# Kernel optimization log

Hardware: AMD Instinct MI355X
Metric: run time of the kernel (lower is better)

The kernel has to match this reference:

```python
import math
import jax, jax.numpy as jnp
import numpy as np

B, N, E, R = 1024, 200, 256, 256

def _layernorm(x, g, b, eps=1e-5):
    mu = x.mean(-1, keepdims=True)
    var = ((x - mu) ** 2).mean(-1, keepdims=True)
    return (x - mu) / jnp.sqrt(var + eps) * g + b

def setup_inputs() -> dict:
    key = jax.random.key(0)
    ks = jax.random.split(key, 16)
    d = {}
    d["e_emb"] = jax.random.normal(ks[0], (B, E), jnp.float32)
    d["nb_rel"] = jax.random.normal(ks[1], (B, N, R), jnp.float32)
    d["delta_t"] = jax.random.uniform(ks[2], (B, N), jnp.float32) * 10.0
    d["r_emb"] = jax.random.normal(ks[3], (B, R), jnp.float32)
    d["hist_mask"] = jax.random.randint(ks[4], (B, N), 0, 2).astype(bool)
    d["rel_w"] = jax.random.normal(ks[5], (E, R), jnp.float32) / math.sqrt(R)
    d["log_tau1"] = jnp.asarray(1.0, jnp.float32)
    d["log_tau2"] = jnp.asarray(2.5, jnp.float32)
    d["sharpness"] = jnp.asarray(1.5, jnp.float32)
    d["log_gamma"] = jnp.asarray(-2.0, jnp.float32)
    d["attn_w"] = jax.random.normal(ks[6], (3, E, E), jnp.float32) / math.sqrt(E)
    d["sp_w"] = jax.random.normal(ks[7], (3, E, 6 * E), jnp.float32) / math.sqrt(6 * E)
    d["sp_b"] = jnp.zeros((3, E), jnp.float32)
    d["ln_g"] = jnp.ones((3, E), jnp.float32)
    d["ln_b"] = jnp.zeros((3, E), jnp.float32)
    d["csq_w"] = jax.random.normal(ks[8], (E, R), jnp.float32) / math.sqrt(R)
    d["csq_b"] = jnp.zeros((E,), jnp.float32)
    d["csl_w"] = jax.random.normal(ks[9], (3, E), jnp.float32) / math.sqrt(E)
    d["csl_b"] = jnp.zeros((3,), jnp.float32)
    d["on_g"] = jnp.ones((E,), jnp.float32)
    d["on_b"] = jnp.zeros((E,), jnp.float32)
    return d

def _pna_one_scale(msgs, mask, e_emb, q_key, attn_w, sp_w, sp_b, ln_g, ln_b):
    # msgs: [B,N,E], mask: [B,N] bool, e_emb: [B,E], q_key: [B,E]
    valid_f = mask[..., None].astype(msgs.dtype)
    n_valid = jnp.maximum(mask.astype(msgs.dtype).sum(1, keepdims=True), 1.0)  # [B,1]
    msgs_v = msgs * valid_f
    mean_v = msgs_v.sum(1) / n_valid
    max_v = msgs_v.max(1)
    min_v = jnp.clip(jnp.where(mask[..., None], msgs, 10000.0).min(1), -10000.0, 10000.0)
    sq_m = (jnp.clip(msgs_v, -10.0, 10.0) ** 2).sum(1) / n_valid
    std_v = jnp.sqrt(jnp.maximum(sq_m - mean_v ** 2, 1e-6))
    q_proj = q_key @ attn_w.T  # [B,E]
    attn_raw = jnp.einsum('bne,be->bn', msgs, q_proj) / math.sqrt(msgs.shape[-1])
    attn_raw = jnp.where(mask, attn_raw, -10000.0)
    all_invalid = ~mask.any(1, keepdims=True)  # [B,1]
    attn_raw = jnp.where(all_invalid, 0.0, attn_raw)
    attn_p = jax.nn.softmax(attn_raw, axis=-1)
    attn_v = jnp.einsum('bn,bne->be', attn_p, msgs)
    feats = jnp.concatenate([mean_v, max_v, min_v, std_v, attn_v, e_emb], axis=-1)  # [B,6E]
    h = feats @ sp_w.T + sp_b
    h = _layernorm(h, ln_g, ln_b)
    return jax.nn.gelu(h, approximate=False)  # dropout = identity (eval mode)

def reference(e_emb, nb_rel, delta_t, r_emb, hist_mask, rel_w, log_tau1, log_tau2,
              sharpness, log_gamma, attn_w, sp_w, sp_b, ln_g, ln_b,
              csq_w, csq_b, csl_w, csl_b, on_g, on_b):
    msgs = jnp.einsum('bnr,er->bne', nb_rel, rel_w)
    gamma = jnp.exp(log_gamma)
    decay = jnp.exp(-gamma * jnp.maximum(delta_t, 0.0))
    msgs_dec = msgs * decay[..., None]
    tau1 = jnp.exp(log_tau1)
    tau2 = jnp.exp(log_tau2) + tau1
    sharp = jnp.clip(sharpness, 0.1, 5.0)
    w_fine = jax.nn.sigmoid(-sharp * (delta_t - tau1))
    w_coarse = jax.nn.sigmoid(sharp * (delta_t - tau2))
    w_mid = jnp.maximum(1.0 - w_fine - w_coarse, 0.0)
    scale_w = jnp.stack([w_fine, w_mid, w_coarse])  # [3,B,N]
    m_scales = msgs_dec[None] * scale_w[..., None]  # [3,B,N,E]
    q_key = r_emb @ rel_w.T  # [B,E]
    pna_v = jax.vmap(_pna_one_scale, in_axes=(0, None, None, None, 0, 0, 0, 0, 0))
    scales = pna_v(m_scales, hist_mask, e_emb, q_key, attn_w, sp_w, sp_b, ln_g, ln_b)  # [3,B,E]
    sq = r_emb @ csq_w.T + csq_b  # [B,E]
    logits = sq @ csl_w.T + csl_b  # [B,3]
    weights = jax.nn.softmax(logits, axis=-1)
    out = jnp.einsum('bs,sbe->be', weights, scales)
    return _layernorm(out, on_g, on_b)  # drop = identity (eval)
```

## Files before the change

### kernel.cpp

```cpp
#include <hip/hip_runtime.h>
#include <math.h>

#define B_   1024
#define N_   200
#define NP_  208
#define E_   256
#define R_   256
#define K6_  1536

typedef __attribute__((ext_vector_type(8))) short bf16x8;
typedef __attribute__((ext_vector_type(4))) float f32x4;

__device__ __forceinline__ unsigned short f2bf(float f) {
  unsigned int u = __float_as_uint(f);
  u += 0x7fffu + ((u >> 16) & 1u);
  return (unsigned short)(u >> 16);
}

__device__ __forceinline__ float gelu_exact(float x) {
  return 0.5f * x * (1.f + erff(x * 0.70710678118654752f));
}

__global__ __launch_bounds__(256) void k_cast(const float* __restrict__ rel_w,
                                              const float* __restrict__ sp_w,
                                              unsigned short* __restrict__ rw_bf,
                                              unsigned short* __restrict__ spw_bf) {
  int idx = blockIdx.x * 256 + threadIdx.x;
  if (idx < E_ * R_) rw_bf[idx] = f2bf(rel_w[idx]);
  int j = idx - E_ * R_;
  if (j >= 0 && j < 3 * E_ * K6_) spw_bf[j] = f2bf(sp_w[j]);
}

__global__ __launch_bounds__(256) void k_qkey(
    const float* __restrict__ r_emb, const float* __restrict__ rel_w,
    const float* __restrict__ csq_w, const float* __restrict__ csq_b,
    const float* __restrict__ csl_w, const float* __restrict__ csl_b,
    float* __restrict__ q_key, float* __restrict__ wts) {
  __shared__ __align__(16) float re[8][256];
  __shared__ __align__(16) float sqs[8][256];
  __shared__ float lg[8][3];
  int b0 = blockIdx.x * 8;
  int tid = threadIdx.x;
  for (int i = tid; i < 8 * 256; i += 256)
    re[i >> 8][i & 255] = r_emb[(size_t)(b0 + (i >> 8)) * 256 + (i & 255)];
  __syncthreads();
  int e = tid;
  float qk[8], sv[8];
#pragma unroll
  for (int i = 0; i < 8; ++i) { qk[i] = 0.f; sv[i] = 0.f; }
  const float4* w4 = (const float4*)(rel_w) + (size_t)e * 64;
  const float4* c4 = (const float4*)(csq_w) + (size_t)e * 64;
  for (int r = 0; r < 64; ++r) {
    float4 w = w4[r];
    float4 c = c4[r];
#pragma unroll
    for (int i = 0; i < 8; ++i) {
      float4 x = ((const float4*)re[i])[r];
      qk[i] += w.x * x.x + w.y * x.y + w.z * x.z + w.w * x.w;
      sv[i] += c.x * x.x + c.y * x.y + c.z * x.z + c.w * x.w;
    }
  }
  float cb = csq_b[e];
#pragma unroll
  for (int i = 0; i < 8; ++i) {
    q_key[(size_t)(b0 + i) * 256 + e] = qk[i];
    sqs[i][e] = sv[i] + cb;
  }
  __syncthreads();
  if (tid < 24) {
    int i = tid / 3, k = tid % 3;
    float acc = csl_b[k];
    for (int ee = 0; ee < 256; ++ee) acc += sqs[i][ee] * csl_w[k * 256 + ee];
    lg[i][k] = acc;
  }
  __syncthreads();
  if (tid < 8) {
    float l0 = lg[tid][0], l1 = lg[tid][1], l2 = lg[tid][2];
    float m = fmaxf(l0, fmaxf(l1, l2));
    float e0 = expf(l0 - m), e1 = expf(l1 - m), e2 = expf(l2 - m);
    float inv = 1.f / (e0 + e1 + e2);
    wts[(b0 + tid) * 4 + 0] = e0 * inv;
    wts[(b0 + tid) * 4 + 1] = e1 * inv;
    wts[(b0 + tid) * 4 + 2] = e2 * inv;
  }
}

__global__ __launch_bounds__(256) void k_qproj(const float* __restrict__ q_key,
                                               const float* __restrict__ attn_w,
                                               float* __restrict__ q_proj) {
  __shared__ __align__(16) float qk[8][256];
  int s = blockIdx.x >> 7;
  int b0 = (blockIdx.x & 127) * 8;
  int tid = threadIdx.x;
  for (int i = tid; i < 2048; i += 256)
    qk[i >> 8][i & 255] = q_key[(size_t)(b0 + (i >> 8)) * 256 + (i & 255)];
  __syncthreads();
  int e = tid;
  float acc[8];
#pragma unroll
  for (int i = 0; i < 8; ++i) acc[i] = 0.f;
  const float4* a4 = (const float4*)(attn_w) + ((size_t)s * 256 + e) * 64;
  for (int r = 0; r < 64; ++r) {
    float4 w = a4[r];
#pragma unroll
    for (int i = 0; i < 8; ++i) {
      float4 x = ((const float4*)qk[i])[r];
      acc[i] += w.x * x.x + w.y * x.y + w.z * x.z + w.w * x.w;
    }
  }
#pragma unroll
  for (int i = 0; i < 8; ++i)
    q_proj[((size_t)s * B_ + b0 + i) * 256 + e] = acc[i];
}

__global__ __launch_bounds__(256) void k_t(const float* __restrict__ q_proj,
                                           const float* __restrict__ rel_w,
                                           float* __restrict__ t_ws) {
  __shared__ __align__(16) float qp[8][256];
  int s = blockIdx.x >> 7;
  int b0 = (blockIdx.x & 127) * 8;
  int tid = threadIdx.x;
  for (int i = tid; i < 2048; i += 256)
    qp[i >> 8][i & 255] = q_proj[((size_t)s * B_ + b0 + (i >> 8)) * 256 + (i & 255)];
  __syncthreads();
  int r = tid;
  float acc[8];
#pragma unroll
  for (int i = 0; i < 8; ++i) acc[i] = 0.f;
  for (int e = 0; e < 256; ++e) {
    float w = rel_w[(size_t)e * 256 + r];
#pragma unroll
    for (int i = 0; i < 8; ++i) acc[i] = fmaf(qp[i][e], w, acc[i]);
  }
#pragma unroll
  for (int i = 0; i < 8; ++i)
    t_ws[((size_t)s * B_ + b0 + i) * 256 + r] = acc[i];
}

__global__ __launch_bounds__(256, 2) void k1_main(
    const float* __restrict__ nb_rel, const float* __restrict__ delta_t,
    const unsigned char* __restrict__ hm_raw, const float* __restrict__ e_emb,
    const float* __restrict__ p_lt1, const float* __restrict__ p_lt2,
    const float* __restrict__ p_sh, const float* __restrict__ p_lgm,
    const unsigned short* __restrict__ rw_bf, const float* __restrict__ t_ws,
    float* __restrict__ feats) {
  __shared__ __align__(16) struct {
    unsigned int a[64 * 132];
    float t[3][256];
    float c[3][NP_];
    float p[3][NP_];
    float maskf[NP_];
  } sm;
  int b = blockIdx.x;
  int tid = threadIdx.x;
  int lane = tid & 63, wave = tid >> 6;
  int row16 = lane & 15, quad = lane >> 4;

  int hasNZoff = 0, hasFP = 0;
  {
    unsigned char c0 = hm_raw[tid];
    unsigned char c1 = hm_raw[256 + tid];
    if ((tid & 3) != 0 && c0 != 0) {
      hasNZoff = 1;
      if (c0 == 0x3Fu || c0 == 0x80u) hasFP = 1;
    }
    if (((256 + tid) & 3) != 0 && c1 != 0) {
      hasNZoff = 1;
      if (c1 == 0x3Fu || c1 == 0x80u) hasFP = 1;
    }
  }
  int cntNZ = __syncthreads_count(hasNZoff);
  int cntFP = __syncthreads_count(hasFP);
  int mmode = (cntNZ == 0) ? 0 : (cntFP > 0 ? 2 : 1);

  float tau1 = expf(p_lt1[0]);
  float tau2 = expf(p_lt2[0]) + tau1;
  float sharp = fminf(fmaxf(p_sh[0], 0.1f), 5.0f);
  float gamma = expf(p_lgm[0]);

  bool mk = false;
  if (tid < NP_) {
    float mf = 0.f, c0 = 0.f, c1 = 0.f, c2 = 0.f;
    if (tid < N_) {
      size_t mi = (size_t)b * N_ + tid;
      if (mmode == 0)      mk = ((const int*)hm_raw)[mi] != 0;
      else if (mmode == 1) mk = hm_raw[mi] != 0;
      else                 mk = ((const float*)hm_raw)[mi] != 0.f;
      float dt = delta_t[mi];
      mf = mk ? 1.f : 0.f;
      float decay = expf(-gamma * fmaxf(dt, 0.f));
      float wf = 1.f / (1.f + expf(sharp * (dt - tau1)));
      float wc = 1.f / (1.f + expf(-sharp * (dt - tau2)));
      float wm = fmaxf(1.f - wf - wc, 0.f);
      c0 = decay * wf; c1 = decay * wm; c2 = decay * wc;
    }
    sm.maskf[tid] = mf;
    sm.c[0][tid] = c0; sm.c[1][tid] = c1; sm.c[2][tid] = c2;
  }
  for (int i = tid; i < 768; i += 256)
    ((float*)sm.t)[i] = t_ws[((size_t)(i >> 8) * B_ + b) * 256 + (i & 255)];

  int cnt = __syncthreads_count(mk ? 1 : 0);
  float nvf = fmaxf((float)cnt, 1.f);
  bool allinv = (cnt == 0);

  if (tid < NP_) {
    if (tid < N_) {
      const float4* row = (const float4*)(nb_rel + ((size_t)b * N_ + tid) * 256);
      const float4* t0 = (const float4*)sm.t[0];
      const float4* t1 = (const float4*)sm.t[1];
      const float4* t2p = (const float4*)sm.t[2];
      float a0 = 0.f, a1 = 0.f, a2 = 0.f;
      for (int r = 0; r < 64; ++r) {
        float4 x = row[r];
        float4 u;
        u = t0[r];  a0 += x.x * u.x + x.y * u.y + x.z * u.z + x.w * u.w;
        u = t1[r];  a1 += x.x * u.x + x.y * u.y + x.z * u.z + x.w * u.w;
        u = t2p[r]; a2 += x.x * u.x + x.y * u.y + x.z * u.z + x.w * u.w;
      }
      bool mkk = sm.maskf[tid] > 0.5f;
      float l0 = sm.c[0][tid] * a0 * 0.0625f;
      float l1 = sm.c[1][tid] * a1 * 0.0625f;
      float l2 = sm.c[2][tid] * a2 * 0.0625f;
      l0 = mkk ? l0 : -1e4f; l1 = mkk ? l1 : -1e4f; l2 = mkk ? l2 : -1e4f;
      if (allinv) { l0 = 0.f; l1 = 0.f; l2 = 0.f; }
      sm.p[0][tid] = l0; sm.p[1][tid] = l1; sm.p[2][tid] = l2;
    } else {
      sm.p[0][tid] = -1e30f; sm.p[1][tid] = -1e30f; sm.p[2][tid] = -1e30f;
    }
  }
  __syncthreads();

  if (wave == 3) {
    for (int i = lane; i < 256; i += 64) {
      float v = e_emb[(size_t)b * 256 + i];
      feats[((size_t)0 * B_ + b) * K6_ + 1280 + i] = v;
      feats[((size_t)1 * B_ + b) * K6_ + 1280 + i] = v;
      feats[((size_t)2 * B_ + b) * K6_ + 1280 + i] = v;
    }
  } else {
    int s = wave;
    float m = -1e30f;
    for (int n = lane; n < NP_; n += 64) m = fmaxf(m, sm.p[s][n]);
#pragma unroll
    for (int o = 32; o >= 1; o >>= 1) m = fmaxf(m, __shfl_xor(m, o, 64));
    float ssum = 0.f;
    for (int n = lane; n < NP_; n += 64) ssum += expf(sm.p[s][n] - m);
#pragma unroll
    for (int o = 32; o >= 1; o >>= 1) ssum += __shfl_xor(ssum, o, 64);
    float inv = 1.f / ssum;
    for (int n = lane; n < NP_; n += 64) sm.p[s][n] = expf(sm.p[s][n] - m) * inv;
  }

  int ebase = wave * 64;
  float s_mean[3][4], s_mx[3][4], s_mn[3][4], s_sq[3][4], s_av[3][4];
#pragma unroll
  for (int s = 0; s < 3; ++s)
#pragma unroll
    for (int t = 0; t < 4; ++t) {
      s_mean[s][t] = 0.f; s_mx[s][t] = -1e30f; s_mn[s][t] = 1e30f;
      s_sq[s][t] = 0.f; s_av[s][t] = 0.f;
    }

  for (int st = 0; st < 4; ++st) {
    int n0 = st * 64;
    int ntc = (st < 3) ? 4 : 1;
    __syncthreads();
    int nf4 = ntc * 16 * 64;
    for (int j = tid; j < nf4; j += 256) {
      int nl = j >> 6;
      int rr = (j & 63) << 2;
      int n = n0 + nl;
      int gn = (n < N_) ? n : (N_ - 1);
      float4 x = *(const float4*)(nb_rel + ((size_t)b * N_ + gn) * 256 + rr);
      unsigned int lo = (unsigned int)f2bf(x.x) | ((unsigned int)f2bf(x.y) << 16);
      unsigned int hi = (unsigned int)f2bf(x.z) | ((unsigned int)f2bf(x.w) << 16);
      int di = nl * 132 + (rr >> 1);
      sm.a[di] = lo;
      sm.a[di + 1] = hi;
    }
    __syncthreads();
    f32x4 acc[4][4];
#pragma unroll
    for (int nt = 0; nt < 4; ++nt)
#pragma unroll
      for (int t = 0; t < 4; ++t)
#pragma unroll
        for (int cc = 0; cc < 4; ++cc) acc[nt][t][cc] = 0.f;
#pragma unroll
    for (int ks = 0; ks < 8; ++ks) {
      bf16x8 bfr[4];
#pragma unroll
      for (int t = 0; t < 4; ++t) {
        int e = ebase + t * 16 + row16;
        int k = ks * 32 + quad * 8;
        bfr[t] = *(const bf16x8*)(rw_bf + (size_t)e * 256 + k);
      }
#pragma unroll
      for (int nt = 0; nt < 4; ++nt) {
        if (nt < ntc) {
          bf16x8 af = *(const bf16x8*)&sm.a[(nt * 16 + row16) * 132 + ks * 16 + quad * 4];
#pragma unroll
          for (int t = 0; t < 4; ++t)
            acc[nt][t] = __builtin_amdgcn_mfma_f32_16x16x32_bf16(af, bfr[t], acc[nt][t], 0, 0, 0);
        }
      }
    }
    for (int nt = 0; nt < 4; ++nt) {
      if (nt < ntc) {
#pragma unroll
        for (int rg = 0; rg < 4; ++rg) {
          int n = n0 + nt * 16 + quad * 4 + rg;
          float mf = sm.maskf[n];
          bool mb = mf > 0.5f;
#pragma unroll
          for (int s = 0; s < 3; ++s) {
            float cs = sm.c[s][n];
            float ps = sm.p[s][n];
#pragma unroll
            for (int t = 0; t < 4; ++t) {
              float msg = acc[nt][t][rg];
              float v = cs * msg;
              float vm = mb ? v : 0.f;
              s_mean[s][t] += vm;
              s_mx[s][t] = fmaxf(s_mx[s][t], vm);
              s_mn[s][t] = fminf(s_mn[s][t], mb ? v : 1e4f);
              float cv = fminf(fmaxf(vm, -10.f), 10.f);
              s_sq[s][t] = fmaf(cv, cv, s_sq[s][t]);
              s_av[s][t] = fmaf(ps, v, s_av[s][t]);
            }
          }
        }
      }
    }
  }
#pragma unroll
  for (int s = 0; s < 3; ++s) {
#pragma unroll
    for (int t = 0; t < 4; ++t) {
      float vmean = s_mean[s][t];
      vmean += __shfl_xor(vmean, 16, 64); vmean += __shfl_xor(vmean, 32, 64);
      float vmx = s_mx[s][t];
      vmx = fmaxf(vmx, __shfl_xor(vmx, 16, 64)); vmx = fmaxf(vmx, __shfl_xor(vmx, 32, 64));
      float vmn = s_mn[s][t];
      vmn = fminf(vmn, __shfl_xor(vmn, 16, 64)); vmn = fminf(vmn, __shfl_xor(vmn, 32, 64));
      float vsq = s_sq[s][t];
      vsq += __shfl_xor(vsq, 16, 64); vsq += __shfl_xor(vsq, 32, 64);
      float vav = s_av[s][t];
      vav += __shfl_xor(vav, 16, 64); vav += __shfl_xor(vav, 32, 64);
      if (lane < 16) {
        int e = ebase + t * 16 + lane;
        size_t base = ((size_t)s * B_ + b) * K6_;
        float meanv = vmean / nvf;
        float stdv = sqrtf(fmaxf(vsq / nvf - meanv * meanv, 1e-6f));
        float mnv = fminf(fmaxf(vmn, -1e4f), 1e4f);
        feats[base + e] = meanv;
        feats[base + 256 + e] = vmx;
        feats[base + 512 + e] = mnv;
        feats[base + 768 + e] = stdv;
        feats[base + 1024 + e] = vav;
      }
    }
  }
}

__global__ __launch_bounds__(256) void k2_kernel(
    const float* __restrict__ feats, const unsigned short* __restrict__ spw_bf,
    const float* __restrict__ sp_b, const float* __restrict__ ln_g,
    const float* __restrict__ ln_b, float* __restrict__ scales) {
  __shared__ __align__(16) union {
    unsigned int a[32 * 132];
    float h[32 * 260];
  } sm;
  int s = blockIdx.x >> 5;
  int b0 = (blockIdx.x & 31) * 32;
  int tid = threadIdx.x, lane = tid & 63, wave = tid >> 6;
  int row16 = lane & 15, quad = lane >> 4;
  int ebase = wave * 64;
  f32x4 acc[2][4];
#pragma unroll
  for (int mt = 0; mt < 2; ++mt)
#pragma unroll
    for (int t = 0; t < 4; ++t)
#pragma unroll
      for (int cc = 0; cc < 4; ++cc) acc[mt][t][cc] = 0.f;

  for (int kc = 0; kc < 6; ++kc) {
    __syncthreads();
    for (int j = tid; j < 2048; j += 256) {
      int rw = j >> 6;
      int kk = (j & 63) << 2;
      float4 x = *(const float4*)(feats + ((size_t)s * B_ + b0 + rw) * K6_ + kc * 256 + kk);
      unsigned int lo = (unsigned int)f2bf(x.x) | ((unsigned int)f2bf(x.y) << 16);
      unsigned int hi = (unsigned int)f2bf(x.z) | ((unsigned int)f2bf(x.w) << 16);
      int di = rw * 132 + (kk >> 1);
      sm.a[di] = lo;
      sm.a[di + 1] = hi;
    }
    __syncthreads();
#pragma unroll
    for (int ks = 0; ks < 8; ++ks) {
      bf16x8 bfr[4];
#pragma unroll
      for (int t = 0; t < 4; ++t) {
        int e = ebase + t * 16 + row16;
        int k = kc * 256 + ks * 32 + quad * 8;
        bfr[t] = *(const bf16x8*)(spw_bf + ((size_t)s * E_ + e) * K6_ + k);
      }
#pragma unroll
      for (int mt = 0; mt < 2; ++mt) {
        bf16x8 af = *(const bf16x8*)&sm.a[(mt * 16 + row16) * 132 + ks * 16 + quad * 4];
#pragma unroll
        for (int t = 0; t < 4; ++t)
          acc[mt][t] = __builtin_amdgcn_mfma_f32_16x16x32_bf16(af, bfr[t], acc[mt][t], 0, 0, 0);
      }
    }
  }
  __syncthreads();
#pragma unroll
  for (int mt = 0; mt < 2; ++mt)
#pragma unroll
    for (int t = 0; t < 4; ++t)
#pragma unroll
      for (int rg = 0; rg < 4; ++rg) {
        int rw = mt * 16 + quad * 4 + rg;
        int e = ebase + t * 16 + row16;
        sm.h[rw * 260 + e] = acc[mt][t][rg] + sp_b[s * 256 + e];
      }
  __syncthreads();
  for (int rr = 0; rr < 8; ++rr) {
    int rw = wave * 8 + rr;
    float4 x = *(const float4*)&sm.h[rw * 260 + lane * 4];
    float sum = x.x + x.y + x.z + x.w;
    float sq = x.x * x.x + x.y * x.y + x.z * x.z + x.w * x.w;
#pragma unroll
    for (int o = 32; o >= 1; o >>= 1) {
      sum += __shfl_xor(sum, o, 64);
      sq += __shfl_xor(sq, o, 64);
    }
    float mu = sum * (1.f / 256.f);
    float var = sq * (1.f / 256.f) - mu * mu;
    float rstd = rsqrtf(var + 1e-5f);
    float4 g = *(const float4*)(ln_g + s * 256 + lane * 4);
    float4 bb = *(const float4*)(ln_b + s * 256 + lane * 4);
    float4 o4;
    o4.x = gelu_exact((x.x - mu) * rstd * g.x + bb.x);
    o4.y = gelu_exact((x.y - mu) * rstd * g.y + bb.y);
    o4.z = gelu_exact((x.z - mu) * rstd * g.z + bb.z);
    o4.w = gelu_exact((x.w - mu) * rstd * g.w + bb.w);
    *(float4*)(scales + ((size_t)s * B_ + b0 + rw) * 256 + lane * 4) = o4;
  }
}

__global__ __launch_bounds__(256) void k3_kernel(
    const float* __restrict__ scales, const float* __restrict__ wts,
    const float* __restrict__ on_g, const float* __restrict__ on_b,
    float* __restrict__ out) {
  __shared__ float rs[4], rq[4];
  int b = blockIdx.x, tid = threadIdx.x, lane = tid & 63, wave = tid >> 6;
  float w0 = wts[b * 4 + 0], w1 = wts[b * 4 + 1], w2 = wts[b * 4 + 2];
  float o = w0 * scales[((size_t)0 * B_ + b) * 256 + tid] +
            w1 * scales[((size_t)1 * B_ + b) * 256 + tid] +
            w2 * scales[((size_t)2 * B_ + b) * 256 + tid];
  float sum = o, sq = o * o;
#pragma unroll
  for (int off = 32; off >= 1; off >>= 1) {
    sum += __shfl_xor(sum, off, 64);
    sq += __shfl_xor(sq, off, 64);
  }
  if (lane == 0) { rs[wave] = sum; rq[wave] = sq; }
  __syncthreads();
  float ts = rs[0] + rs[1] + rs[2] + rs[3];
  float tq = rq[0] + rq[1] + rq[2] + rq[3];
  float mu = ts * (1.f / 256.f);
  float var = tq * (1.f / 256.f) - mu * mu;
  float rstd = rsqrtf(var + 1e-5f);
  out[(size_t)b * 256 + tid] = (o - mu) * rstd * on_g[tid] + on_b[tid];
}

extern "C" void kernel_launch(void* const* d_in, const int* in_sizes, int n_in,
                              void* d_out, int out_size, void* d_ws, size_t ws_size,
                              hipStream_t stream) {
  const float* e_emb   = (const float*)d_in[0];
  const float* nb_rel  = (const float*)d_in[1];
  const float* delta_t = (const float*)d_in[2];
  const float* r_emb   = (const float*)d_in[3];
  const unsigned char* hist_mask = (const unsigned char*)d_in[4];
  const float* rel_w   = (const float*)d_in[5];
  const float* lt1     = (const float*)d_in[6];
  const float* lt2     = (const float*)d_in[7];
  const float* shp     = (const float*)d_in[8];
  const float* lgm     = (const float*)d_in[9];
  const float* attn_w  = (const float*)d_in[10];
  const float* sp_w    = (const float*)d_in[11];
  const float* sp_b    = (const float*)d_in[12];
  const float* ln_g    = (const float*)d_in[13];
  const float* ln_b    = (const float*)d_in[14];
  const float* csq_w   = (const float*)d_in[15];
  const float* csq_b   = (const float*)d_in[16];
  const float* csl_w   = (const float*)d_in[17];
  const float* csl_b   = (const float*)d_in[18];
  const float* on_g    = (const float*)d_in[19];
  const float* on_b    = (const float*)d_in[20];
  float* out = (float*)d_out;

  char* ws = (char*)d_ws;
  unsigned short* rw_bf  = (unsigned short*)(ws + 0);
  unsigned short* spw_bf = (unsigned short*)(ws + 131072);
  float* q_key  = (float*)(ws + 2490368);
  float* q_proj = (float*)(ws + 3538944);
  float* t_ws   = (float*)(ws + 6684672);
  float* wts    = (float*)(ws + 9830400);
  float* feats  = (float*)(ws + 9846784);
  float* scales = (float*)(ws + 28721152);

  hipLaunchKernelGGL(k_cast, dim3(4864), dim3(256), 0, stream, rel_w, sp_w, rw_bf, spw_bf);
  hipLaunchKernelGGL(k_qkey, dim3(128), dim3(256), 0, stream, r_emb, rel_w, csq_w, csq_b,
                     csl_w, csl_b, q_key, wts);
  hipLaunchKernelGGL(k_qproj, dim3(384), dim3(256), 0, stream, q_key, attn_w, q_proj);
  hipLaunchKernelGGL(k_t, dim3(384), dim3(256), 0, stream, q_proj, rel_w, t_ws);
  hipLaunchKernelGGL(k1_main, dim3(1024), dim3(256), 0, stream, nb_rel, delta_t, hist_mask,
                     e_emb, lt1, lt2, shp, lgm, rw_bf, t_ws, feats);
  hipLaunchKernelGGL(k2_kernel, dim3(96), dim3(256), 0, stream, feats, spw_bf, sp_b,
                     ln_g, ln_b, scales);
  hipLaunchKernelGGL(k3_kernel, dim3(1024), dim3(256), 0, stream, scales, wts, on_g, on_b, out);
}
```

Measured before the change: 582.8 us.

## Restructure k1_main to read nb_rel once with 512 threads and bf16 feats

k1_main now runs 512 threads per block and streams each nb_rel row through registers only once. The attention dot products against the t vectors are computed with wave shuffles while the same row is packed to bf16 into a full-size shared tile. Before, the kernel read nb_rel twice: once for the attention logits and once for the MFMA staging. Each wave now keeps its rel_w fragment in registers across all 13 row tiles, and the mask and offset handling is folded into precomputed per-row metadata. The feats buffer is written as bf16, which halves its traffic and lets k2 copy tiles straight into shared memory without converting. The costs are a larger shared-memory footprint that may limit occupancy, higher register pressure, and bf16 rounding applied to the pooled features before they are stored.

Result: faster. 537.8 us (-7.7%).

```diff
diff --git a/kernel.cpp b/kernel.cpp
--- a/kernel.cpp
+++ b/kernel.cpp
@@ -3,7 +3,8 @@
 
 #define B_   1024
 #define N_   200
-#define NP_  208
+#define NR_  208
+#define NT_  13
 #define E_   256
 #define R_   256
 #define K6_  1536
@@ -137,36 +138,35 @@
     t_ws[((size_t)s * B_ + b0 + i) * 256 + r] = acc[i];
 }
 
-__global__ __launch_bounds__(256, 2) void k1_main(
+__global__ __launch_bounds__(512, 2) void k1_main(
     const float* __restrict__ nb_rel, const float* __restrict__ delta_t,
     const unsigned char* __restrict__ hm_raw, const float* __restrict__ e_emb,
     const float* __restrict__ p_lt1, const float* __restrict__ p_lt2,
     const float* __restrict__ p_sh, const float* __restrict__ p_lgm,
     const unsigned short* __restrict__ rw_bf, const float* __restrict__ t_ws,
-    float* __restrict__ feats) {
+    unsigned short* __restrict__ feats) {
   __shared__ __align__(16) struct {
-    unsigned int a[64 * 132];
-    float t[3][256];
-    float c[3][NP_];
-    float p[3][NP_];
-    float maskf[NP_];
+    unsigned int a[NR_ * 132];
+    float araw[3][NR_];
+    float c[3][NR_];
+    float p[3][NR_];
+    float nmeta[NR_][9];
   } sm;
   int b = blockIdx.x;
   int tid = threadIdx.x;
   int lane = tid & 63, wave = tid >> 6;
   int row16 = lane & 15, quad = lane >> 4;
 
+  float4 tf0 = *(const float4*)&t_ws[((size_t)0 * B_ + b) * 256 + lane * 4];
+  float4 tf1 = *(const float4*)&t_ws[((size_t)1 * B_ + b) * 256 + lane * 4];
+  float4 tf2 = *(const float4*)&t_ws[((size_t)2 * B_ + b) * 256 + lane * 4];
+
   int hasNZoff = 0, hasFP = 0;
   {
-    unsigned char c0 = hm_raw[tid];
-    unsigned char c1 = hm_raw[256 + tid];
-    if ((tid & 3) != 0 && c0 != 0) {
+    unsigned char cc = hm_raw[tid];
+    if ((tid & 3) != 0 && cc != 0) {
       hasNZoff = 1;
-      if (c0 == 0x3Fu || c0 == 0x80u) hasFP = 1;
-    }
-    if (((256 + tid) & 3) != 0 && c1 != 0) {
-      hasNZoff = 1;
-      if (c1 == 0x3Fu || c1 == 0x80u) hasFP = 1;
+      if (cc == 0x3Fu || cc == 0x80u) hasFP = 1;
     }
   }
   int cntNZ = __syncthreads_count(hasNZoff);
@@ -179,7 +179,7 @@
   float gamma = expf(p_lgm[0]);
 
   bool mk = false;
-  if (tid < NP_) {
+  if (tid < NR_) {
     float mf = 0.f, c0 = 0.f, c1 = 0.f, c2 = 0.f;
     if (tid < N_) {
       size_t mi = (size_t)b * N_ + tid;
@@ -194,150 +194,148 @@
       float wm = fmaxf(1.f - wf - wc, 0.f);
       c0 = decay * wf; c1 = decay * wm; c2 = decay * wc;
     }
-    sm.maskf[tid] = mf;
     sm.c[0][tid] = c0; sm.c[1][tid] = c1; sm.c[2][tid] = c2;
-  }
-  for (int i = tid; i < 768; i += 256)
-    ((float*)sm.t)[i] = t_ws[((size_t)(i >> 8) * B_ + b) * 256 + (i & 255)];
-
+    sm.nmeta[tid][0] = mf * c0;
+    sm.nmeta[tid][1] = mf * c1;
+    sm.nmeta[tid][2] = mf * c2;
+    sm.nmeta[tid][3] = mk ? 0.f : 1e4f;
+    sm.nmeta[tid][7] = mf;
+  }
   int cnt = __syncthreads_count(mk ? 1 : 0);
   float nvf = fmaxf((float)cnt, 1.f);
   bool allinv = (cnt == 0);
 
-  if (tid < NP_) {
+  {
+    const float* src = nb_rel + (size_t)b * N_ * 256;
+    int n0 = wave;
+    int g0 = (n0 < N_) ? n0 : (N_ - 1);
+    float4 x = *(const float4*)(src + (size_t)g0 * 256 + lane * 4);
+    for (int i = 0; i < 26; ++i) {
+      int ncur = i * 8 + wave;
+      float4 xn;
+      if (i < 25) {
+        int nn = (i + 1) * 8 + wave;
+        int gn = (nn < N_) ? nn : (N_ - 1);
+        xn = *(const float4*)(src + (size_t)gn * 256 + lane * 4);
+      }
+      float d0 = x.x * tf0.x + x.y * tf0.y + x.z * tf0.z + x.w * tf0.w;
+      float d1 = x.x * tf1.x + x.y * tf1.y + x.z * tf1.z + x.w * tf1.w;
+      float d2 = x.x * tf2.x + x.y * tf2.y + x.z * tf2.z + x.w * tf2.w;
+#pragma unroll
+      for (int o = 1; o < 64; o <<= 1) {
+        d0 += __shfl_xor(d0, o, 64);
+        d1 += __shfl_xor(d1, o, 64);
+        d2 += __shfl_xor(d2, o, 64);
+      }
+      if (lane < 3) sm.araw[lane][ncur] = (lane == 0) ? d0 : ((lane == 1) ? d1 : d2);
+      uint2 pk;
+      pk.x = (unsigned int)f2bf(x.x) | ((unsigned int)f2bf(x.y) << 16);
+      pk.y = (unsigned int)f2bf(x.z) | ((unsigned int)f2bf(x.w) << 16);
+      *(uint2*)&sm.a[ncur * 132 + lane * 2] = pk;
+      x = xn;
+    }
+  }
+
+  bf16x8 bfr[2][8];
+#pragma unroll
+  for (int t = 0; t < 2; ++t) {
+    int e = wave * 32 + t * 16 + row16;
+#pragma unroll
+    for (int ks = 0; ks < 8; ++ks)
+      bfr[t][ks] = *(const bf16x8*)(rw_bf + (size_t)e * 256 + ks * 32 + quad * 8);
+  }
+  __syncthreads();
+
+  if (tid < NR_) {
+    float l0 = -1e30f, l1 = -1e30f, l2 = -1e30f;
     if (tid < N_) {
-      const float4* row = (const float4*)(nb_rel + ((size_t)b * N_ + tid) * 256);
-      const float4* t0 = (const float4*)sm.t[0];
-      const float4* t1 = (const float4*)sm.t[1];
-      const float4* t2p = (const float4*)sm.t[2];
-      float a0 = 0.f, a1 = 0.f, a2 = 0.f;
-      for (int r = 0; r < 64; ++r) {
-        float4 x = row[r];
-        float4 u;
-        u = t0[r];  a0 += x.x * u.x + x.y * u.y + x.z * u.z + x.w * u.w;
-        u = t1[r];  a1 += x.x * u.x + x.y * u.y + x.z * u.z + x.w * u.w;
-        u = t2p[r]; a2 += x.x * u.x + x.y * u.y + x.z * u.z + x.w * u.w;
-      }
-      bool mkk = sm.maskf[tid] > 0.5f;
-      float l0 = sm.c[0][tid] * a0 * 0.0625f;
-      float l1 = sm.c[1][tid] * a1 * 0.0625f;
-      float l2 = sm.c[2][tid] * a2 * 0.0625f;
+      bool mkk = sm.nmeta[tid][7] > 0.5f;
+      l0 = sm.c[0][tid] * sm.araw[0][tid] * 0.0625f;
+      l1 = sm.c[1][tid] * sm.araw[1][tid] * 0.0625f;
+      l2 = sm.c[2][tid] * sm.araw[2][tid] * 0.0625f;
       l0 = mkk ? l0 : -1e4f; l1 = mkk ? l1 : -1e4f; l2 = mkk ? l2 : -1e4f;
       if (allinv) { l0 = 0.f; l1 = 0.f; l2 = 0.f; }
-      sm.p[0][tid] = l0; sm.p[1][tid] = l1; sm.p[2][tid] = l2;
-    } else {
-      sm.p[0][tid] = -1e30f; sm.p[1][tid] = -1e30f; sm.p[2][tid] = -1e30f;
-    }
-  }
-  __syncthreads();
-
-  if (wave == 3) {
+    }
+    sm.p[0][tid] = l0; sm.p[1][tid] = l1; sm.p[2][tid] = l2;
+  }
+  __syncthreads();
+
+  if (wave < 3) {
+    int s = wave;
+    float m = -1e30f;
+    for (int n = lane; n < NR_; n += 64) m = fmaxf(m, sm.p[s][n]);
+#pragma unroll
+    for (int o = 32; o >= 1; o >>= 1) m = fmaxf(m, __shfl_xor(m, o, 64));
+    float ssum = 0.f;
+    for (int n = lane; n < NR_; n += 64) ssum += expf(sm.p[s][n] - m);
+#pragma unroll
+    for (int o = 32; o >= 1; o >>= 1) ssum += __shfl_xor(ssum, o, 64);
+    float inv = 1.f / ssum;
+    for (int n = lane; n < NR_; n += 64) {
+      float pv = expf(sm.p[s][n] - m) * inv;
+      sm.nmeta[n][4 + s] = pv * sm.c[s][n];
+    }
+  } else if (wave == 3) {
     for (int i = lane; i < 256; i += 64) {
-      float v = e_emb[(size_t)b * 256 + i];
+      unsigned short v = f2bf(e_emb[(size_t)b * 256 + i]);
       feats[((size_t)0 * B_ + b) * K6_ + 1280 + i] = v;
       feats[((size_t)1 * B_ + b) * K6_ + 1280 + i] = v;
       feats[((size_t)2 * B_ + b) * K6_ + 1280 + i] = v;
     }
-  } else {
-    int s = wave;
-    float m = -1e30f;
-    for (int n = lane; n < NP_; n += 64) m = fmaxf(m, sm.p[s][n]);
-#pragma unroll
-    for (int o = 32; o >= 1; o >>= 1) m = fmaxf(m, __shfl_xor(m, o, 64));
-    float ssum = 0.f;
-    for (int n = lane; n < NP_; n += 64) ssum += expf(sm.p[s][n] - m);
-#pragma unroll
-    for (int o = 32; o >= 1; o >>= 1) ssum += __shfl_xor(ssum, o, 64);
-    float inv = 1.f / ssum;
-    for (int n = lane; n < NP_; n += 64) sm.p[s][n] = expf(sm.p[s][n] - m) * inv;
-  }
-
-  int ebase = wave * 64;
-  float s_mean[3][4], s_mx[3][4], s_mn[3][4], s_sq[3][4], s_av[3][4];
+  }
+  __syncthreads();
+
+  float s_mean[3][2], s_mx[3][2], s_mn[3][2], s_sq[3][2], s_av[3][2];
 #pragma unroll
   for (int s = 0; s < 3; ++s)
 #pragma unroll
-    for (int t = 0; t < 4; ++t) {
+    for (int t = 0; t < 2; ++t) {
       s_mean[s][t] = 0.f; s_mx[s][t] = -1e30f; s_mn[s][t] = 1e30f;
       s_sq[s][t] = 0.f; s_av[s][t] = 0.f;
     }
 
-  for (int st = 0; st < 4; ++st) {
-    int n0 = st * 64;
-    int ntc = (st < 3) ? 4 : 1;
-    __syncthreads();
-    int nf4 = ntc * 16 * 64;
-    for (int j = tid; j < nf4; j += 256) {
-      int nl = j >> 6;
-      int rr = (j & 63) << 2;
-      int n = n0 + nl;
-      int gn = (n < N_) ? n : (N_ - 1);
-      float4 x = *(const float4*)(nb_rel + ((size_t)b * N_ + gn) * 256 + rr);
-      unsigned int lo = (unsigned int)f2bf(x.x) | ((unsigned int)f2bf(x.y) << 16);
-      unsigned int hi = (unsigned int)f2bf(x.z) | ((unsigned int)f2bf(x.w) << 16);
-      int di = nl * 132 + (rr >> 1);
-      sm.a[di] = lo;
-      sm.a[di + 1] = hi;
-    }
-    __syncthreads();
-    f32x4 acc[4][4];
-#pragma unroll
-    for (int nt = 0; nt < 4; ++nt)
-#pragma unroll
-      for (int t = 0; t < 4; ++t)
-#pragma unroll
-        for (int cc = 0; cc < 4; ++cc) acc[nt][t][cc] = 0.f;
+  for (int nt = 0; nt < NT_; ++nt) {
+    f32x4 acc[2];
+#pragma unroll
+    for (int t = 0; t < 2; ++t)
+#pragma unroll
+      for (int cc = 0; cc < 4; ++cc) acc[t][cc] = 0.f;
 #pragma unroll
     for (int ks = 0; ks < 8; ++ks) {
-      bf16x8 bfr[4];
-#pragma unroll
-      for (int t = 0; t < 4; ++t) {
-        int e = ebase + t * 16 + row16;
-        int k = ks * 32 + quad * 8;
-        bfr[t] = *(const bf16x8*)(rw_bf + (size_t)e * 256 + k);
-      }
-#pragma unroll
-      for (int nt = 0; nt < 4; ++nt) {
-        if (nt < ntc) {
-          bf16x8 af = *(const bf16x8*)&sm.a[(nt * 16 + row16) * 132 + ks * 16 + quad * 4];
-#pragma unroll
-          for (int t = 0; t < 4; ++t)
-            acc[nt][t] = __builtin_amdgcn_mfma_f32_16x16x32_bf16(af, bfr[t], acc[nt][t], 0, 0, 0);
+      bf16x8 af = *(const bf16x8*)&sm.a[(nt * 16 + row16) * 132 + ks * 16 + quad * 4];
+      acc[0] = __builtin_amdgcn_mfma_f32_16x16x32_bf16(af, bfr[0][ks], acc[0], 0, 0, 0);
+      acc[1] = __builtin_amdgcn_mfma_f32_16x16x32_bf16(af, bfr[1][ks], acc[1], 0, 0, 0);
+    }
+    int nb = nt * 16 + quad * 4;
+#pragma unroll
+    for (int rg = 0; rg < 4; ++rg) {
+      int n = nb + rg;
+      float cmv[3], qv[3];
+      cmv[0] = sm.nmeta[n][0]; cmv[1] = sm.nmeta[n][1]; cmv[2] = sm.nmeta[n][2];
+      float off = sm.nmeta[n][3];
+      qv[0] = sm.nmeta[n][4]; qv[1] = sm.nmeta[n][5]; qv[2] = sm.nmeta[n][6];
+#pragma unroll
+      for (int t = 0; t < 2; ++t) {
+        float m = acc[t][rg];
+#pragma unroll
+        for (int s = 0; s < 3; ++s) {
+          float vm = cmv[s] * m;
+          s_mean[s][t] += vm;
+          s_mx[s][t] = fmaxf(s_mx[s][t], vm);
+          float mnc = fmaf(cmv[s], m, off);
+          s_mn[s][t] = fminf(s_mn[s][t], mnc);
+          float cv = fminf(fmaxf(vm, -10.f), 10.f);
+          s_sq[s][t] = fmaf(cv, cv, s_sq[s][t]);
+          s_av[s][t] = fmaf(qv[s], m, s_av[s][t]);
         }
       }
     }
-    for (int nt = 0; nt < 4; ++nt) {
-      if (nt < ntc) {
-#pragma unroll
-        for (int rg = 0; rg < 4; ++rg) {
-          int n = n0 + nt * 16 + quad * 4 + rg;
-          float mf = sm.maskf[n];
-          bool mb = mf > 0.5f;
-#pragma unroll
-          for (int s = 0; s < 3; ++s) {
-            float cs = sm.c[s][n];
-            float ps = sm.p[s][n];
-#pragma unroll
-            for (int t = 0; t < 4; ++t) {
-              float msg = acc[nt][t][rg];
-              float v = cs * msg;
-              float vm = mb ? v : 0.f;
-              s_mean[s][t] += vm;
-              s_mx[s][t] = fmaxf(s_mx[s][t], vm);
-              s_mn[s][t] = fminf(s_mn[s][t], mb ? v : 1e4f);
-              float cv = fminf(fmaxf(vm, -10.f), 10.f);
-              s_sq[s][t] = fmaf(cv, cv, s_sq[s][t]);
-              s_av[s][t] = fmaf(ps, v, s_av[s][t]);
-            }
-          }
-        }
-      }
-    }
-  }
+  }
+
 #pragma unroll
   for (int s = 0; s < 3; ++s) {
 #pragma unroll
-    for (int t = 0; t < 4; ++t) {
+    for (int t = 0; t < 2; ++t) {
       float vmean = s_mean[s][t];
       vmean += __shfl_xor(vmean, 16, 64); vmean += __shfl_xor(vmean, 32, 64);
       float vmx = s_mx[s][t];
@@ -349,23 +347,23 @@
       float vav = s_av[s][t];
       vav += __shfl_xor(vav, 16, 64); vav += __shfl_xor(vav, 32, 64);
       if (lane < 16) {
-        int e = ebase + t * 16 + lane;
+        int e = wave * 32 + t * 16 + lane;
         size_t base = ((size_t)s * B_ + b) * K6_;
         float meanv = vmean / nvf;
         float stdv = sqrtf(fmaxf(vsq / nvf - meanv * meanv, 1e-6f));
         float mnv = fminf(fmaxf(vmn, -1e4f), 1e4f);
-        feats[base + e] = meanv;
-        feats[base + 256 + e] = vmx;
-        feats[base + 512 + e] = mnv;
-        feats[base + 768 + e] = stdv;
-        feats[base + 1024 + e] = vav;
+        feats[base + e] = f2bf(meanv);
+        feats[base + 256 + e] = f2bf(vmx);
+        feats[base + 512 + e] = f2bf(mnv);
+        feats[base + 768 + e] = f2bf(stdv);
+        feats[base + 1024 + e] = f2bf(vav);
       }
     }
   }
 }
 
 __global__ __launch_bounds__(256) void k2_kernel(
-    const float* __restrict__ feats, const unsigned short* __restrict__ spw_bf,
+    const unsigned short* __restrict__ feats, const unsigned short* __restrict__ spw_bf,
     const float* __restrict__ sp_b, const float* __restrict__ ln_g,
     const float* __restrict__ ln_b, float* __restrict__ scales) {
   __shared__ __align__(16) union {
@@ -387,15 +385,10 @@
 
   for (int kc = 0; kc < 6; ++kc) {
     __syncthreads();
-    for (int j = tid; j < 2048; j += 256) {
-      int rw = j >> 6;
-      int kk = (j & 63) << 2;
-      float4 x = *(const float4*)(feats + ((size_t)s * B_ + b0 + rw) * K6_ + kc * 256 + kk);
-      unsigned int lo = (unsigned int)f2bf(x.x) | ((unsigned int)f2bf(x.y) << 16);
-      unsigned int hi = (unsigned int)f2bf(x.z) | ((unsigned int)f2bf(x.w) << 16);
-      int di = rw * 132 + (kk >> 1);
-      sm.a[di] = lo;
-      sm.a[di + 1] = hi;
+    for (int j = tid; j < 1024; j += 256) {
+      int rw = j >> 5, ck = j & 31;
+      bf16x8 v = *(const bf16x8*)(feats + ((size_t)s * B_ + b0 + rw) * K6_ + kc * 256 + ck * 8);
+      *(bf16x8*)((unsigned short*)&sm.a[rw * 132] + ck * 8) = v;
     }
     __syncthreads();
 #pragma unroll
@@ -511,15 +504,15 @@
   float* q_proj = (float*)(ws + 3538944);
   float* t_ws   = (float*)(ws + 6684672);
   float* wts    = (float*)(ws + 9830400);
-  float* feats  = (float*)(ws + 9846784);
-  float* scales = (float*)(ws + 28721152);
+  unsigned short* feats = (unsigned short*)(ws + 9846784);
+  float* scales = (float*)(ws + 19283968);
 
   hipLaunchKernelGGL(k_cast, dim3(4864), dim3(256), 0, stream, rel_w, sp_w, rw_bf, spw_bf);
   hipLaunchKernelGGL(k_qkey, dim3(128), dim3(256), 0, stream, r_emb, rel_w, csq_w, csq_b,
                      csl_w, csl_b, q_key, wts);
   hipLaunchKernelGGL(k_qproj, dim3(384), dim3(256), 0, stream, q_key, attn_w, q_proj);
   hipLaunchKernelGGL(k_t, dim3(384), dim3(256), 0, stream, q_proj, rel_w, t_ws);
-  hipLaunchKernelGGL(k1_main, dim3(1024), dim3(256), 0, stream, nb_rel, delta_t, hist_mask,
+  hipLaunchKernelGGL(k1_main, dim3(1024), dim3(512), 0, stream, nb_rel, delta_t, hist_mask,
                      e_emb, lt1, lt2, shp, lgm, rw_bf, t_ws, feats);
   hipLaunchKernelGGL(k2_kernel, dim3(96), dim3(256), 0, stream, feats, spw_bf, sp_b,
                      ln_g, ln_b, scales);
```
